# Performance work log

Measured on AMD Instinct MI355X. Metric: run time of the kernel, lower is better.

## Reference

```python
import jax, jax.numpy as jnp
import numpy as np

# dims
B, S, D, DS = 4, 4096, 2048, 64
NF, NR, NT = 4096, 2048, 2048  # feature / relational / transfer neuron pools
KF, KR, KT = 8, 4, 6           # top-k per pool


def setup_inputs() -> dict:
    key = jax.random.key(0)
    k1, k2, k3, k4 = jax.random.split(key, 4)
    x = jax.random.normal(k1, (B, S, D), dtype=jnp.float32)
    importance = jax.random.uniform(k2, (B, S), dtype=jnp.float32)
    proj_w = jax.random.normal(k3, (D, DS), dtype=jnp.float32) * 0.02
    proj_b = jnp.zeros((DS,), dtype=jnp.float32)
    neuron_emb = jax.random.normal(k4, (NF + NR + NT, DS), dtype=jnp.float32) * 0.02
    return {"x": x, "importance": importance, "proj_w": proj_w,
            "proj_b": proj_b, "neuron_emb": neuron_emb}


def _topk_sparsify(w, k):
    # top-k along last dim, scatter back, renormalize (matches _topk_sparsify)
    vals, idx = jax.lax.top_k(w, k)                      # [B,k]
    rows = jnp.arange(w.shape[0])[:, None]
    sparse = jnp.zeros_like(w).at[rows, idx].set(vals)   # [B,N]
    return sparse / (sparse.sum(axis=-1, keepdims=True) + 1e-8)


def reference(x, importance, proj_w, proj_b, neuron_emb):
    # eval mode: dropout off, no excitability bias, no aux loss
    h = x @ proj_w + proj_b                               # [B,S,DS]
    norm = jnp.maximum(jnp.linalg.norm(neuron_emb, axis=-1, keepdims=True), 1e-12)
    emb = neuron_emb / norm                               # F.normalize
    logits = jnp.einsum('bsd,nd->bsn', h, emb)            # [B,S,NF+NR+NT]

    feat_pref = jax.nn.softmax(logits[..., :NF], axis=-1)
    relQ_pref = jax.nn.softmax(logits[..., NF:NF + NR], axis=-1)
    relK_pref = jax.nn.softmax(logits[..., NF:NF + NR], axis=-1)
    tran_pref = jax.nn.softmax(logits[..., NF + NR:], axis=-1)

    # importance-weighted pooling over tokens -> dense per-batch routing weights
    fw = _topk_sparsify(jnp.einsum('bs,bsn->bn', importance, feat_pref), KF)
    qw = _topk_sparsify(jnp.einsum('bs,bsn->bn', importance, relQ_pref), KR)
    kw = _topk_sparsify(jnp.einsum('bs,bsn->bn', importance, relK_pref), KR)
    tw = _topk_sparsify(jnp.einsum('bs,bsn->bn', importance, tran_pref), KT)

    return jnp.concatenate([fw, qw, kw, tw], axis=-1)     # [B, NF+2*NR+NT]
```

## Files before the change

### kernel.cpp

```cpp
#include <hip/hip_runtime.h>
#include <math.h>

#define BATCH 4
#define SEQ   4096
#define DIM   2048
#define DS    64
#define NF    4096
#define NR    2048
#define NT    2048
#define NTOT  8192
#define TOK   16384
#define KSPLIT 8
#define KS    (DIM / KSPLIT)

typedef __attribute__((ext_vector_type(8))) __bf16 bf16x8;
typedef __attribute__((ext_vector_type(4))) float  f32x4;

static __device__ __forceinline__ unsigned short f2bf(float x) {
  unsigned int u = __float_as_uint(x);
  u += 0x7fffu + ((u >> 16) & 1u);
  return (unsigned short)(u >> 16);
}
static __device__ __forceinline__ float bf2f(unsigned int lo16) {
  return __uint_as_float(lo16 << 16);
}

static __device__ __forceinline__ void split8(const float4& a, const float4& b,
                                              bf16x8& hi, bf16x8& lo) {
  float v[8] = {a.x, a.y, a.z, a.w, b.x, b.y, b.z, b.w};
  union { unsigned short u[8]; bf16x8 v8; } H, L;
#pragma unroll
  for (int i = 0; i < 8; ++i) {
    unsigned short h = f2bf(v[i]);
    H.u[i] = h;
    L.u[i] = f2bf(v[i] - bf2f(h));
  }
  hi = H.v8; lo = L.v8;
}

__global__ __launch_bounds__(256) void k_prep(const float* __restrict__ emb,
                                              const float* __restrict__ W,
                                              unsigned short* __restrict__ eh,
                                              unsigned short* __restrict__ el,
                                              unsigned short* __restrict__ wth,
                                              unsigned short* __restrict__ wtl) {
  if (blockIdx.x < NTOT / 4) {
    int row  = blockIdx.x * 4 + (threadIdx.x >> 6);
    int lane = threadIdx.x & 63;
    float v  = emb[(size_t)row * DS + lane];
    float ss = v * v;
#pragma unroll
    for (int m = 32; m >= 1; m >>= 1) ss += __shfl_xor(ss, m, 64);
    float sc = 1.0f / fmaxf(sqrtf(ss), 1e-12f);
    float w  = v * sc;
    unsigned short hi = f2bf(w);
    eh[(size_t)row * DS + lane] = hi;
    el[(size_t)row * DS + lane] = f2bf(w - bf2f(hi));
  } else {
    int c = blockIdx.x - NTOT / 4;
#pragma unroll
    for (int it = 0; it < 8; ++it) {
      int k = threadIdx.x + it * 256;
      float v = W[(size_t)k * DS + c];
      unsigned short hi = f2bf(v);
      wth[(size_t)c * DIM + k] = hi;
      wtl[(size_t)c * DIM + k] = f2bf(v - bf2f(hi));
    }
  }
}

__global__ __launch_bounds__(512) void k_h(
    const float* __restrict__ x, const unsigned short* __restrict__ wth,
    const unsigned short* __restrict__ wtl, float* __restrict__ Hpart) {
  __shared__ __align__(16) unsigned short wsh[64 * KS];
  __shared__ __align__(16) unsigned short wsl[64 * KS];
  const int tid   = threadIdx.x;
  const int t0    = blockIdx.x * 128;
  const int kbase = blockIdx.y * KS;
  const int lane  = tid & 63, wv = tid >> 6;
  const int fr    = lane & 15, oct = lane >> 4;

#pragma unroll
  for (int it = 0; it < 4; ++it) {
    int idx = tid + it * 512;
    int c = idx >> 5, k16 = idx & 31;
    int bo = (c * 512 + k16 * 16) ^ ((c & 7) << 4);
    size_t src = ((size_t)c * DIM + kbase) * 2 + (size_t)k16 * 16;
    *reinterpret_cast<uint4*>((char*)wsh + bo) =
        *reinterpret_cast<const uint4*>((const char*)wth + src);
    *reinterpret_cast<uint4*>((char*)wsl + bo) =
        *reinterpret_cast<const uint4*>((const char*)wtl + src);
  }
  __syncthreads();

  const float* xp = x + (size_t)(t0 + wv * 16 + fr) * DIM + kbase + oct * 8;

  f32x4 acc[4];
#pragma unroll
  for (int j = 0; j < 4; ++j) acc[j] = (f32x4)0.0f;

  float4 xa = *reinterpret_cast<const float4*>(xp);
  float4 xb = *reinterpret_cast<const float4*>(xp + 4);

#pragma unroll
  for (int s = 0; s < KS / 32; ++s) {
    bf16x8 ah, al;
    split8(xa, xb, ah, al);
    if (s + 1 < KS / 32) {
      xa = *reinterpret_cast<const float4*>(xp + (s + 1) * 32);
      xb = *reinterpret_cast<const float4*>(xp + (s + 1) * 32 + 4);
    }
#pragma unroll
    for (int j = 0; j < 4; ++j) {
      int col = j * 16 + fr;
      int bo = (col * 512 + s * 64 + oct * 16) ^ ((col & 7) << 4);
      bf16x8 bh = *reinterpret_cast<const bf16x8*>((const char*)wsh + bo);
      bf16x8 bl = *reinterpret_cast<const bf16x8*>((const char*)wsl + bo);
      acc[j] = __builtin_amdgcn_mfma_f32_16x16x32_bf16(ah, bh, acc[j], 0, 0, 0);
      acc[j] = __builtin_amdgcn_mfma_f32_16x16x32_bf16(ah, bl, acc[j], 0, 0, 0);
      acc[j] = __builtin_amdgcn_mfma_f32_16x16x32_bf16(al, bh, acc[j], 0, 0, 0);
    }
  }

  float* op = Hpart + (size_t)blockIdx.y * TOK * DS;
#pragma unroll
  for (int j = 0; j < 4; ++j) {
    int c = j * 16 + fr;
#pragma unroll
    for (int r = 0; r < 4; ++r) {
      int t = t0 + wv * 16 + oct * 4 + r;
      op[(size_t)t * DS + c] = acc[j][r];
    }
  }
}

__global__ __launch_bounds__(256) void k_hc(const float* __restrict__ Hpart,
                                            const float* __restrict__ bias,
                                            unsigned short* __restrict__ hh,
                                            unsigned short* __restrict__ hl) {
  int idx = blockIdx.x * 256 + threadIdx.x;
  int t = idx >> 4, q = idx & 15;
  size_t o = (size_t)t * DS + q * 4;
  float4 bv = *reinterpret_cast<const float4*>(&bias[q * 4]);
  float v0 = bv.x, v1 = bv.y, v2 = bv.z, v3 = bv.w;
#pragma unroll
  for (int p = 0; p < KSPLIT; ++p) {
    float4 s = *reinterpret_cast<const float4*>(&Hpart[(size_t)p * TOK * DS + o]);
    v0 += s.x; v1 += s.y; v2 += s.z; v3 += s.w;
  }
  unsigned short h0 = f2bf(v0), h1 = f2bf(v1), h2 = f2bf(v2), h3 = f2bf(v3);
  uint2 hi; hi.x = h0 | ((unsigned)h1 << 16); hi.y = h2 | ((unsigned)h3 << 16);
  uint2 lo;
  lo.x = (unsigned)f2bf(v0 - bf2f(h0)) | ((unsigned)f2bf(v1 - bf2f(h1)) << 16);
  lo.y = (unsigned)f2bf(v2 - bf2f(h2)) | ((unsigned)f2bf(v3 - bf2f(h3)) << 16);
  *reinterpret_cast<uint2*>(&hh[o]) = hi;
  *reinterpret_cast<uint2*>(&hl[o]) = lo;
}

template<int MODE>
__global__ __launch_bounds__(256, 4) void k_zle(
    const unsigned short* __restrict__ hh, const unsigned short* __restrict__ hl,
    const unsigned short* __restrict__ eh, const unsigned short* __restrict__ el,
    const float* __restrict__ a, float* __restrict__ Zp, float* __restrict__ Bp) {
  __shared__ __align__(16) unsigned short esh[128 * 64];
  __shared__ __align__(16) unsigned short esl[128 * 64];
  __shared__ float red2[512];
  const int tid = threadIdx.x;
  const int tg  = blockIdx.x;
  const int cb  = blockIdx.y;
  const int n0  = cb * 128;

#pragma unroll
  for (int it = 0; it < 4; ++it) {
    int idx = tid + it * 256;
    int r = idx >> 3, k8 = idx & 7;
    int bo = (r * 128 + k8 * 16) ^ ((r & 7) << 4);
    *reinterpret_cast<uint4*>((char*)esh + bo) =
        *reinterpret_cast<const uint4*>((const char*)eh + (size_t)(n0 + r) * 128 + k8 * 16);
    *reinterpret_cast<uint4*>((char*)esl + bo) =
        *reinterpret_cast<const uint4*>((const char*)el + (size_t)(n0 + r) * 128 + k8 * 16);
  }
  if (MODE == 2) { red2[tid] = 0.0f; red2[256 + tid] = 0.0f; }
  __syncthreads();

  const int lane = tid & 63;
  const int wv   = tid >> 6;
  const int fr   = lane & 15;
  const int oct  = lane >> 4;
  const int sl   = (cb < 32) ? 0 : ((cb < 48) ? 1 : 2);

#pragma unroll 1
  for (int it = 0; it < 8; ++it) {
    const int tbase = tg * 1024 + it * 128 + wv * 32;

    bf16x8 ah[2][2], al[2][2];
#pragma unroll
    for (int i = 0; i < 2; ++i)
#pragma unroll
      for (int kh = 0; kh < 2; ++kh) {
        size_t off = (size_t)(tbase + i * 16 + fr) * DS + kh * 32 + oct * 8;
        ah[i][kh] = *reinterpret_cast<const bf16x8*>(hh + off);
        al[i][kh] = *reinterpret_cast<const bf16x8*>(hl + off);
      }

    float av[2][4];
    if (MODE == 2) {
#pragma unroll
      for (int i = 0; i < 2; ++i)
#pragma unroll
        for (int r = 0; r < 4; ++r)
          av[i][r] = a[(size_t)sl * TOK + tbase + i * 16 + oct * 4 + r];
    }
    float rs[2][4];
    if (MODE == 0) {
#pragma unroll
      for (int i = 0; i < 2; ++i)
#pragma unroll
        for (int r = 0; r < 4; ++r) rs[i][r] = 0.0f;
    }

#pragma unroll 1
    for (int jq = 0; jq < 2; ++jq) {
      f32x4 acc[2][4];
#pragma unroll
      for (int i = 0; i < 2; ++i)
#pragma unroll
        for (int j = 0; j < 4; ++j) acc[i][j] = (f32x4)0.0f;

#pragma unroll
      for (int j = 0; j < 4; ++j) {
        int col = (jq * 4 + j) * 16 + fr;
        bf16x8 bh[2], bl[2];
#pragma unroll
        for (int kh = 0; kh < 2; ++kh) {
          int bo = (col * 128 + (kh * 32 + oct * 8) * 2) ^ ((col & 7) << 4);
          bh[kh] = *reinterpret_cast<const bf16x8*>((const char*)esh + bo);
          bl[kh] = *reinterpret_cast<const bf16x8*>((const char*)esl + bo);
        }
#pragma unroll
        for (int i = 0; i < 2; ++i) {
#pragma unroll
          for (int kh = 0; kh < 2; ++kh) {
            acc[i][j] = __builtin_amdgcn_mfma_f32_16x16x32_bf16(ah[i][kh], bh[kh], acc[i][j], 0, 0, 0);
            acc[i][j] = __builtin_amdgcn_mfma_f32_16x16x32_bf16(ah[i][kh], bl[kh], acc[i][j], 0, 0, 0);
            acc[i][j] = __builtin_amdgcn_mfma_f32_16x16x32_bf16(al[i][kh], bh[kh], acc[i][j], 0, 0, 0);
          }
        }
      }

      if (MODE == 0) {
#pragma unroll
        for (int i = 0; i < 2; ++i)
#pragma unroll
          for (int j = 0; j < 4; ++j)
#pragma unroll
            for (int r = 0; r < 4; ++r) rs[i][r] += __expf(acc[i][j][r]);
      } else {
#pragma unroll
        for (int j = 0; j < 4; ++j) {
          float s = 0.0f;
#pragma unroll
          for (int i = 0; i < 2; ++i)
#pragma unroll
            for (int r = 0; r < 4; ++r)
              s = fmaf(av[i][r], __expf(acc[i][j][r]), s);
          s += __shfl_xor(s, 16, 64);
          s += __shfl_xor(s, 32, 64);
          if (oct == 0)
            red2[wv * 128 + (jq * 4 + j) * 16 + fr] += s;
        }
      }
    }

    if (MODE == 0) {
#pragma unroll
      for (int m = 1; m < 16; m <<= 1)
#pragma unroll
        for (int i = 0; i < 2; ++i)
#pragma unroll
          for (int r = 0; r < 4; ++r) rs[i][r] += __shfl_xor(rs[i][r], m, 64);
      if (fr == 0) {
#pragma unroll
        for (int i = 0; i < 2; ++i)
#pragma unroll
          for (int r = 0; r < 4; ++r) {
            int t = tbase + i * 16 + oct * 4 + r;
            Zp[(size_t)t * 64 + cb] = rs[i][r];
          }
      }
    }
  }

  if (MODE == 2) {
    __syncthreads();
    if (tid < 128) {
      float v = red2[tid] + red2[128 + tid] + red2[256 + tid] + red2[384 + tid];
      Bp[(size_t)tg * NTOT + n0 + tid] = v;
    }
  }
}

__global__ __launch_bounds__(256) void k_a2(const float* __restrict__ Zp,
                                            const float* __restrict__ imp,
                                            float* __restrict__ a) {
  int t = blockIdx.x * 256 + threadIdx.x;
  const float4* zp = reinterpret_cast<const float4*>(&Zp[(size_t)t * 64]);
  float zf = 0.f, zr = 0.f, zt = 0.f;
#pragma unroll
  for (int q = 0; q < 8; ++q)  { float4 v = zp[q]; zf += (v.x + v.y) + (v.z + v.w); }
#pragma unroll
  for (int q = 8; q < 12; ++q) { float4 v = zp[q]; zr += (v.x + v.y) + (v.z + v.w); }
#pragma unroll
  for (int q = 12; q < 16; ++q){ float4 v = zp[q]; zt += (v.x + v.y) + (v.z + v.w); }
  float im = imp[t];
  a[t]           = im / zf;
  a[TOK + t]     = im / zr;
  a[2 * TOK + t] = im / zt;
}

__global__ __launch_bounds__(256) void k_red(const float* __restrict__ Bp,
                                             float* __restrict__ pooled) {
  int idx = blockIdx.x * 256 + threadIdx.x;
  int b = idx >> 13;
  int n = idx & (NTOT - 1);
  const float* src = Bp + (size_t)(b * 4) * NTOT + n;
  float s = 0.0f;
#pragma unroll
  for (int g = 0; g < 4; ++g) s += src[(size_t)g * NTOT];
  pooled[idx] = s;
}

__global__ __launch_bounds__(256) void k_topk(const float* __restrict__ pooled,
                                              float* __restrict__ out) {
  __shared__ float p[4096];
  __shared__ float rv[256];
  __shared__ int   ri[256];
  __shared__ float vals[8];
  __shared__ int   idxs[8];
  __shared__ float s_inv;

  const int bid = blockIdx.x;
  const int b   = bid / 3;
  const int sl  = bid % 3;
  const int off = (sl == 0) ? 0 : ((sl == 1) ? NF : NF + NR);
  const int N   = (sl == 0) ? NF : NR;
  const int K   = (sl == 0) ? 8 : ((sl == 1) ? 4 : 6);
  const int tid = threadIdx.x;

  for (int i = tid; i < N; i += 256)
    p[i] = pooled[(size_t)b * NTOT + off + i];
  __syncthreads();

  for (int k = 0; k < K; ++k) {
    float bv = -2.0f;
    int bi = 1 << 30;
    for (int i = tid; i < N; i += 256) {
      float v = p[i];
      if (v > bv) { bv = v; bi = i; }
    }
    rv[tid] = bv; ri[tid] = bi;
    __syncthreads();
    for (int st = 128; st > 0; st >>= 1) {
      if (tid < st) {
        float v2 = rv[tid + st]; int i2 = ri[tid + st];
        if (v2 > rv[tid] || (v2 == rv[tid] && i2 < ri[tid])) {
          rv[tid] = v2; ri[tid] = i2;
        }
      }
      __syncthreads();
    }
    if (tid == 0) {
      vals[k] = rv[0]; idxs[k] = ri[0];
      p[ri[0]] = -1.0f;
    }
    __syncthreads();
  }

  if (tid == 0) {
    float s = 0.0f;
    for (int k = 0; k < K; ++k) s += vals[k];
    s_inv = 1.0f / (s + 1e-8f);
  }
  __syncthreads();

  float* ob = out + (size_t)b * (NF + 2 * NR + NT);
  if (sl == 0) {
    for (int i = tid; i < NF; i += 256) ob[i] = 0.0f;
  } else if (sl == 1) {
    for (int i = tid; i < NR; i += 256) { ob[NF + i] = 0.0f; ob[NF + NR + i] = 0.0f; }
  } else {
    for (int i = tid; i < NT; i += 256) ob[NF + 2 * NR + i] = 0.0f;
  }
  __syncthreads();
  if (tid < K) {
    float v = vals[tid] * s_inv;
    int ix = idxs[tid];
    if (sl == 0) {
      ob[ix] = v;
    } else if (sl == 1) {
      ob[NF + ix] = v;
      ob[NF + NR + ix] = v;
    } else {
      ob[NF + 2 * NR + ix] = v;
    }
  }
}

extern "C" void kernel_launch(void* const* d_in, const int* in_sizes, int n_in,
                              void* d_out, int out_size, void* d_ws, size_t ws_size,
                              hipStream_t stream) {
  const float* x    = (const float*)d_in[0];
  const float* imp  = (const float*)d_in[1];
  const float* W    = (const float*)d_in[2];
  const float* bias = (const float*)d_in[3];
  const float* emb  = (const float*)d_in[4];
  float* out = (float*)d_out;

  unsigned short* eh  = (unsigned short*)d_ws;
  unsigned short* el  = eh  + (size_t)NTOT * DS;
  unsigned short* wth = el  + (size_t)NTOT * DS;
  unsigned short* wtl = wth + (size_t)DS * DIM;
  unsigned short* hh  = wtl + (size_t)DS * DIM;
  unsigned short* hl  = hh  + (size_t)TOK * DS;
  float* Zp     = (float*)(hl + (size_t)TOK * DS);
  float* a      = Zp + (size_t)TOK * 64;
  float* Bp     = a + 3 * (size_t)TOK;
  float* pooled = Bp + (size_t)16 * NTOT;
  float* Hpart  = pooled + (size_t)BATCH * NTOT;

  size_t need = (2 * (size_t)NTOT * DS + 2 * (size_t)DS * DIM +
                 2 * (size_t)TOK * DS) * sizeof(unsigned short) +
                ((size_t)TOK * 64 + 3 * (size_t)TOK + 16 * (size_t)NTOT +
                 (size_t)BATCH * NTOT + (size_t)KSPLIT * TOK * DS) * sizeof(float);
  if (ws_size < need) return;

  k_prep<<<NTOT / 4 + DS, 256, 0, stream>>>(emb, W, eh, el, wth, wtl);
  k_h<<<dim3(TOK / 128, KSPLIT), 512, 0, stream>>>(x, wth, wtl, Hpart);
  k_hc<<<TOK * 16 / 256, 256, 0, stream>>>(Hpart, bias, hh, hl);

  k_zle<0><<<dim3(16, 64), 256, 0, stream>>>(hh, hl, eh, el, nullptr, Zp, nullptr);
  k_a2<<<TOK / 256, 256, 0, stream>>>(Zp, imp, a);
  k_zle<2><<<dim3(16, 64), 256, 0, stream>>>(hh, hl, eh, el, a, nullptr, Bp);
  k_red<<<(BATCH * NTOT) / 256, 256, 0, stream>>>(Bp, pooled);
  k_topk<<<12, 256, 0, stream>>>(pooled, out);
}
```

Baseline: 164.0 us.

## Fuse two logit passes and normalizer into one cooperative kernel with grid syncs

Replaces the three launches (partition-function pass, per-token scale computation, weighted pooling pass) with a single cooperative kernel that stages the embedding tile in LDS once and uses grid-wide syncs between phases. This removes two kernel launch gaps and the second LDS staging of embeddings. It relies on all 1024 blocks being co-resident (4 blocks/CU on 256 CUs); if the cooperative launch fails, it falls back to the old three-kernel path. Grid syncs add their own barrier cost, and the per-token scale phase runs on only 64 blocks while the rest wait.

```diff
diff --git a/kernel.cpp b/kernel.cpp
--- a/kernel.cpp
+++ b/kernel.cpp
@@ -1,4 +1,5 @@
 #include <hip/hip_runtime.h>
+#include <hip/hip_cooperative_groups.h>
 #include <math.h>
 
 #define BATCH 4
@@ -157,6 +158,220 @@
   *reinterpret_cast<uint2*>(&hl[o]) = lo;
 }
 
+static __device__ __forceinline__ void stage_e(
+    const unsigned short* __restrict__ eh, const unsigned short* __restrict__ el,
+    unsigned short* esh, unsigned short* esl, int n0, int tid) {
+#pragma unroll
+  for (int it = 0; it < 4; ++it) {
+    int idx = tid + it * 256;
+    int r = idx >> 3, k8 = idx & 7;
+    int bo = (r * 128 + k8 * 16) ^ ((r & 7) << 4);
+    *reinterpret_cast<uint4*>((char*)esh + bo) =
+        *reinterpret_cast<const uint4*>((const char*)eh + (size_t)(n0 + r) * 128 + k8 * 16);
+    *reinterpret_cast<uint4*>((char*)esl + bo) =
+        *reinterpret_cast<const uint4*>((const char*)el + (size_t)(n0 + r) * 128 + k8 * 16);
+  }
+}
+
+static __device__ __forceinline__ void passA(
+    const unsigned short* __restrict__ hh, const unsigned short* __restrict__ hl,
+    const unsigned short* esh, const unsigned short* esl,
+    float* __restrict__ Zp, int tg, int cb, int tid) {
+  const int lane = tid & 63, wv = tid >> 6;
+  const int fr = lane & 15, oct = lane >> 4;
+
+#pragma unroll 1
+  for (int it = 0; it < 8; ++it) {
+    const int tbase = tg * 1024 + it * 128 + wv * 32;
+    bf16x8 ah[2][2], al[2][2];
+#pragma unroll
+    for (int i = 0; i < 2; ++i)
+#pragma unroll
+      for (int kh = 0; kh < 2; ++kh) {
+        size_t off = (size_t)(tbase + i * 16 + fr) * DS + kh * 32 + oct * 8;
+        ah[i][kh] = *reinterpret_cast<const bf16x8*>(hh + off);
+        al[i][kh] = *reinterpret_cast<const bf16x8*>(hl + off);
+      }
+    float rs[2][4];
+#pragma unroll
+    for (int i = 0; i < 2; ++i)
+#pragma unroll
+      for (int r = 0; r < 4; ++r) rs[i][r] = 0.0f;
+
+#pragma unroll 1
+    for (int jq = 0; jq < 2; ++jq) {
+      f32x4 acc[2][4];
+#pragma unroll
+      for (int i = 0; i < 2; ++i)
+#pragma unroll
+        for (int j = 0; j < 4; ++j) acc[i][j] = (f32x4)0.0f;
+#pragma unroll
+      for (int j = 0; j < 4; ++j) {
+        int col = (jq * 4 + j) * 16 + fr;
+        bf16x8 bh[2], bl[2];
+#pragma unroll
+        for (int kh = 0; kh < 2; ++kh) {
+          int bo = (col * 128 + (kh * 32 + oct * 8) * 2) ^ ((col & 7) << 4);
+          bh[kh] = *reinterpret_cast<const bf16x8*>((const char*)esh + bo);
+          bl[kh] = *reinterpret_cast<const bf16x8*>((const char*)esl + bo);
+        }
+#pragma unroll
+        for (int i = 0; i < 2; ++i) {
+#pragma unroll
+          for (int kh = 0; kh < 2; ++kh) {
+            acc[i][j] = __builtin_amdgcn_mfma_f32_16x16x32_bf16(ah[i][kh], bh[kh], acc[i][j], 0, 0, 0);
+            acc[i][j] = __builtin_amdgcn_mfma_f32_16x16x32_bf16(ah[i][kh], bl[kh], acc[i][j], 0, 0, 0);
+            acc[i][j] = __builtin_amdgcn_mfma_f32_16x16x32_bf16(al[i][kh], bh[kh], acc[i][j], 0, 0, 0);
+          }
+        }
+      }
+#pragma unroll
+      for (int i = 0; i < 2; ++i)
+#pragma unroll
+        for (int j = 0; j < 4; ++j)
+#pragma unroll
+          for (int r = 0; r < 4; ++r) rs[i][r] += __expf(acc[i][j][r]);
+    }
+
+#pragma unroll
+    for (int m = 1; m < 16; m <<= 1)
+#pragma unroll
+      for (int i = 0; i < 2; ++i)
+#pragma unroll
+        for (int r = 0; r < 4; ++r) rs[i][r] += __shfl_xor(rs[i][r], m, 64);
+    if (fr == 0) {
+#pragma unroll
+      for (int i = 0; i < 2; ++i)
+#pragma unroll
+        for (int r = 0; r < 4; ++r) {
+          int t = tbase + i * 16 + oct * 4 + r;
+          Zp[(size_t)t * 64 + cb] = rs[i][r];
+        }
+    }
+  }
+}
+
+static __device__ __forceinline__ void passB(
+    const unsigned short* __restrict__ hh, const unsigned short* __restrict__ hl,
+    const unsigned short* esh, const unsigned short* esl,
+    const float* __restrict__ a, float* red2, float* __restrict__ Bp,
+    int tg, int cb, int tid) {
+  const int lane = tid & 63, wv = tid >> 6;
+  const int fr = lane & 15, oct = lane >> 4;
+  const int n0 = cb * 128;
+  const int sl = (cb < 32) ? 0 : ((cb < 48) ? 1 : 2);
+
+#pragma unroll 1
+  for (int it = 0; it < 8; ++it) {
+    const int tbase = tg * 1024 + it * 128 + wv * 32;
+    bf16x8 ah[2][2], al[2][2];
+#pragma unroll
+    for (int i = 0; i < 2; ++i)
+#pragma unroll
+      for (int kh = 0; kh < 2; ++kh) {
+        size_t off = (size_t)(tbase + i * 16 + fr) * DS + kh * 32 + oct * 8;
+        ah[i][kh] = *reinterpret_cast<const bf16x8*>(hh + off);
+        al[i][kh] = *reinterpret_cast<const bf16x8*>(hl + off);
+      }
+    float av[2][4];
+#pragma unroll
+    for (int i = 0; i < 2; ++i)
+#pragma unroll
+      for (int r = 0; r < 4; ++r)
+        av[i][r] = a[(size_t)sl * TOK + tbase + i * 16 + oct * 4 + r];
+
+#pragma unroll 1
+    for (int jq = 0; jq < 2; ++jq) {
+      f32x4 acc[2][4];
+#pragma unroll
+      for (int i = 0; i < 2; ++i)
+#pragma unroll
+        for (int j = 0; j < 4; ++j) acc[i][j] = (f32x4)0.0f;
+#pragma unroll
+      for (int j = 0; j < 4; ++j) {
+        int col = (jq * 4 + j) * 16 + fr;
+        bf16x8 bh[2], bl[2];
+#pragma unroll
+        for (int kh = 0; kh < 2; ++kh) {
+          int bo = (col * 128 + (kh * 32 + oct * 8) * 2) ^ ((col & 7) << 4);
+          bh[kh] = *reinterpret_cast<const bf16x8*>((const char*)esh + bo);
+          bl[kh] = *reinterpret_cast<const bf16x8*>((const char*)esl + bo);
+        }
+#pragma unroll
+        for (int i = 0; i < 2; ++i) {
+#pragma unroll
+          for (int kh = 0; kh < 2; ++kh) {
+            acc[i][j] = __builtin_amdgcn_mfma_f32_16x16x32_bf16(ah[i][kh], bh[kh], acc[i][j], 0, 0, 0);
+            acc[i][j] = __builtin_amdgcn_mfma_f32_16x16x32_bf16(ah[i][kh], bl[kh], acc[i][j], 0, 0, 0);
+            acc[i][j] = __builtin_amdgcn_mfma_f32_16x16x32_bf16(al[i][kh], bh[kh], acc[i][j], 0, 0, 0);
+          }
+        }
+      }
+#pragma unroll
+      for (int j = 0; j < 4; ++j) {
+        float s = 0.0f;
+#pragma unroll
+        for (int i = 0; i < 2; ++i)
+#pragma unroll
+          for (int r = 0; r < 4; ++r)
+            s = fmaf(av[i][r], __expf(acc[i][j][r]), s);
+        s += __shfl_xor(s, 16, 64);
+        s += __shfl_xor(s, 32, 64);
+        if (oct == 0)
+          red2[wv * 128 + (jq * 4 + j) * 16 + fr] += s;
+      }
+    }
+  }
+
+  __syncthreads();
+  if (tid < 128) {
+    float v = red2[tid] + red2[128 + tid] + red2[256 + tid] + red2[384 + tid];
+    Bp[(size_t)tg * NTOT + n0 + tid] = v;
+  }
+}
+
+__global__ __launch_bounds__(256, 4) void k_zfused(
+    const unsigned short* __restrict__ hh, const unsigned short* __restrict__ hl,
+    const unsigned short* __restrict__ eh, const unsigned short* __restrict__ el,
+    const float* __restrict__ imp, float* __restrict__ Zp,
+    float* __restrict__ a, float* __restrict__ Bp) {
+  __shared__ __align__(16) unsigned short esh[128 * 64];
+  __shared__ __align__(16) unsigned short esl[128 * 64];
+  __shared__ float red2[512];
+  const int tid = threadIdx.x;
+  const int tg  = blockIdx.x;
+  const int cb  = blockIdx.y;
+
+  stage_e(eh, el, esh, esl, cb * 128, tid);
+  red2[tid] = 0.0f; red2[256 + tid] = 0.0f;
+  __syncthreads();
+
+  passA(hh, hl, esh, esl, Zp, tg, cb, tid);
+
+  cooperative_groups::this_grid().sync();
+
+  int flat = blockIdx.y * gridDim.x + blockIdx.x;
+  if (flat < 64) {
+    int t = flat * 256 + tid;
+    const float4* zp = reinterpret_cast<const float4*>(&Zp[(size_t)t * 64]);
+    float zf = 0.f, zr = 0.f, zt = 0.f;
+#pragma unroll
+    for (int q = 0; q < 8; ++q)  { float4 v = zp[q]; zf += (v.x + v.y) + (v.z + v.w); }
+#pragma unroll
+    for (int q = 8; q < 12; ++q) { float4 v = zp[q]; zr += (v.x + v.y) + (v.z + v.w); }
+#pragma unroll
+    for (int q = 12; q < 16; ++q){ float4 v = zp[q]; zt += (v.x + v.y) + (v.z + v.w); }
+    float im = imp[t];
+    a[t]           = im / zf;
+    a[TOK + t]     = im / zr;
+    a[2 * TOK + t] = im / zt;
+  }
+
+  cooperative_groups::this_grid().sync();
+
+  passB(hh, hl, esh, esl, a, red2, Bp, tg, cb, tid);
+}
+
 template<int MODE>
 __global__ __launch_bounds__(256, 4) void k_zle(
     const unsigned short* __restrict__ hh, const unsigned short* __restrict__ hl,
@@ -168,136 +383,11 @@
   const int tid = threadIdx.x;
   const int tg  = blockIdx.x;
   const int cb  = blockIdx.y;
-  const int n0  = cb * 128;
-
-#pragma unroll
-  for (int it = 0; it < 4; ++it) {
-    int idx = tid + it * 256;
-    int r = idx >> 3, k8 = idx & 7;
-    int bo = (r * 128 + k8 * 16) ^ ((r & 7) << 4);
-    *reinterpret_cast<uint4*>((char*)esh + bo) =
-        *reinterpret_cast<const uint4*>((const char*)eh + (size_t)(n0 + r) * 128 + k8 * 16);
-    *reinterpret_cast<uint4*>((char*)esl + bo) =
-        *reinterpret_cast<const uint4*>((const char*)el + (size_t)(n0 + r) * 128 + k8 * 16);
-  }
+  stage_e(eh, el, esh, esl, cb * 128, tid);
   if (MODE == 2) { red2[tid] = 0.0f; red2[256 + tid] = 0.0f; }
   __syncthreads();
-
-  const int lane = tid & 63;
-  const int wv   = tid >> 6;
-  const int fr   = lane & 15;
-  const int oct  = lane >> 4;
-  const int sl   = (cb < 32) ? 0 : ((cb < 48) ? 1 : 2);
-
-#pragma unroll 1
-  for (int it = 0; it < 8; ++it) {
-    const int tbase = tg * 1024 + it * 128 + wv * 32;
-
-    bf16x8 ah[2][2], al[2][2];
-#pragma unroll
-    for (int i = 0; i < 2; ++i)
-#pragma unroll
-      for (int kh = 0; kh < 2; ++kh) {
-        size_t off = (size_t)(tbase + i * 16 + fr) * DS + kh * 32 + oct * 8;
-        ah[i][kh] = *reinterpret_cast<const bf16x8*>(hh + off);
-        al[i][kh] = *reinterpret_cast<const bf16x8*>(hl + off);
-      }
-
-    float av[2][4];
-    if (MODE == 2) {
-#pragma unroll
-      for (int i = 0; i < 2; ++i)
-#pragma unroll
-        for (int r = 0; r < 4; ++r)
-          av[i][r] = a[(size_t)sl * TOK + tbase + i * 16 + oct * 4 + r];
-    }
-    float rs[2][4];
-    if (MODE == 0) {
-#pragma unroll
-      for (int i = 0; i < 2; ++i)
-#pragma unroll
-        for (int r = 0; r < 4; ++r) rs[i][r] = 0.0f;
-    }
-
-#pragma unroll 1
-    for (int jq = 0; jq < 2; ++jq) {
-      f32x4 acc[2][4];
-#pragma unroll
-      for (int i = 0; i < 2; ++i)
-#pragma unroll
-        for (int j = 0; j < 4; ++j) acc[i][j] = (f32x4)0.0f;
-
-#pragma unroll
-      for (int j = 0; j < 4; ++j) {
-        int col = (jq * 4 + j) * 16 + fr;
-        bf16x8 bh[2], bl[2];
-#pragma unroll
-        for (int kh = 0; kh < 2; ++kh) {
-          int bo = (col * 128 + (kh * 32 + oct * 8) * 2) ^ ((col & 7) << 4);
-          bh[kh] = *reinterpret_cast<const bf16x8*>((const char*)esh + bo);
-          bl[kh] = *reinterpret_cast<const bf16x8*>((const char*)esl + bo);
-        }
-#pragma unroll
-        for (int i = 0; i < 2; ++i) {
-#pragma unroll
-          for (int kh = 0; kh < 2; ++kh) {
-            acc[i][j] = __builtin_amdgcn_mfma_f32_16x16x32_bf16(ah[i][kh], bh[kh], acc[i][j], 0, 0, 0);
-            acc[i][j] = __builtin_amdgcn_mfma_f32_16x16x32_bf16(ah[i][kh], bl[kh], acc[i][j], 0, 0, 0);
-            acc[i][j] = __builtin_amdgcn_mfma_f32_16x16x32_bf16(al[i][kh], bh[kh], acc[i][j], 0, 0, 0);
-          }
-        }
-      }
-
-      if (MODE == 0) {
-#pragma unroll
-        for (int i = 0; i < 2; ++i)
-#pragma unroll
-          for (int j = 0; j < 4; ++j)
-#pragma unroll
-            for (int r = 0; r < 4; ++r) rs[i][r] += __expf(acc[i][j][r]);
-      } else {
-#pragma unroll
-        for (int j = 0; j < 4; ++j) {
-          float s = 0.0f;
-#pragma unroll
-          for (int i = 0; i < 2; ++i)
-#pragma unroll
-            for (int r = 0; r < 4; ++r)
-              s = fmaf(av[i][r], __expf(acc[i][j][r]), s);
-          s += __shfl_xor(s, 16, 64);
-          s += __shfl_xor(s, 32, 64);
-          if (oct == 0)
-            red2[wv * 128 + (jq * 4 + j) * 16 + fr] += s;
-        }
-      }
-    }
-
-    if (MODE == 0) {
-#pragma unroll
-      for (int m = 1; m < 16; m <<= 1)
-#pragma unroll
-        for (int i = 0; i < 2; ++i)
-#pragma unroll
-          for (int r = 0; r < 4; ++r) rs[i][r] += __shfl_xor(rs[i][r], m, 64);
-      if (fr == 0) {
-#pragma unroll
-        for (int i = 0; i < 2; ++i)
-#pragma unroll
-          for (int r = 0; r < 4; ++r) {
-            int t = tbase + i * 16 + oct * 4 + r;
-            Zp[(size_t)t * 64 + cb] = rs[i][r];
-          }
-      }
-    }
-  }
-
-  if (MODE == 2) {
-    __syncthreads();
-    if (tid < 128) {
-      float v = red2[tid] + red2[128 + tid] + red2[256 + tid] + red2[384 + tid];
-      Bp[(size_t)tg * NTOT + n0 + tid] = v;
-    }
-  }
+  if (MODE == 0) passA(hh, hl, esh, esl, Zp, tg, cb, tid);
+  else           passB(hh, hl, esh, esl, a, red2, Bp, tg, cb, tid);
 }
 
 __global__ __launch_bounds__(256) void k_a2(const float* __restrict__ Zp,
@@ -438,9 +528,22 @@
   k_h<<<dim3(TOK / 128, KSPLIT), 512, 0, stream>>>(x, wth, wtl, Hpart);
   k_hc<<<TOK * 16 / 256, 256, 0, stream>>>(Hpart, bias, hh, hl);
 
-  k_zle<0><<<dim3(16, 64), 256, 0, stream>>>(hh, hl, eh, el, nullptr, Zp, nullptr);
-  k_a2<<<TOK / 256, 256, 0, stream>>>(Zp, imp, a);
-  k_zle<2><<<dim3(16, 64), 256, 0, stream>>>(hh, hl, eh, el, a, nullptr, Bp);
+  {
+    const unsigned short* hh_c = hh; const unsigned short* hl_c = hl;
+    const unsigned short* eh_c = eh; const unsigned short* el_c = el;
+    const float* imp_c = imp;
+    float* Zp_c = Zp; float* a_c = a; float* Bp_c = Bp;
+    void* args[8] = { &hh_c, &hl_c, &eh_c, &el_c, &imp_c, &Zp_c, &a_c, &Bp_c };
+    hipError_t e = hipLaunchCooperativeKernel(
+        reinterpret_cast<const void*>(k_zfused), dim3(16, 64), dim3(256),
+        args, 0, stream);
+    if (e != hipSuccess) {
+      k_zle<0><<<dim3(16, 64), 256, 0, stream>>>(hh, hl, eh, el, nullptr, Zp, nullptr);
+      k_a2<<<TOK / 256, 256, 0, stream>>>(Zp, imp, a);
+      k_zle<2><<<dim3(16, 64), 256, 0, stream>>>(hh, hl, eh, el, a, nullptr, Bp);
+    }
+  }
+
   k_red<<<(BATCH * NTOT) / 256, 256, 0, stream>>>(Bp, pooled);
   k_topk<<<12, 256, 0, stream>>>(pooled, out);
 }
```

Result: slower. 411.4 us (+150.9%).
